# Optimization experiments

Measured on AMD Instinct MI355X. Metric: run time of the kernel, lower is better.

The kernel has to match this reference:

```python
import jax, jax.numpy as jnp
import numpy as np

B, T, E, H, NH = 8, 1024, 128, 1024, 16
HD = H // NH  # head dim = 64

def _split_heads(x):
    # [B, S, H] -> [B, NH, S, HD]
    b, s, _ = x.shape
    return x.reshape(b, s, NH, HD).transpose(0, 2, 1, 3)

def setup_inputs() -> dict:
    key = jax.random.key(0)
    ks = jax.random.split(key, 16)
    std = 0.02
    inp = {
        "token_hidden_states": jax.random.normal(ks[0], (B, T, H), jnp.float32),
        "entity_hidden_states": jax.random.normal(ks[1], (B, E, H), jnp.float32),
        "attention_mask": jnp.zeros((B, 1, 1, T + E), jnp.float32),
        "query_pos": jax.random.normal(ks[2], (B, E, H), jnp.float32),
        # word q/k/v projections
        "Wq": jax.random.normal(ks[3], (H, H), jnp.float32) * std,
        "bq": jnp.zeros((H,), jnp.float32),
        "Wk": jax.random.normal(ks[4], (H, H), jnp.float32) * std,
        "bk": jnp.zeros((H,), jnp.float32),
        "Wv": jax.random.normal(ks[5], (H, H), jnp.float32) * std,
        "bv": jnp.zeros((H,), jnp.float32),
        # entity-aware e2w q/k/v projections
        "Weq": jax.random.normal(ks[6], (H, H), jnp.float32) * std,
        "beq": jnp.zeros((H,), jnp.float32),
        "Wek": jax.random.normal(ks[7], (H, H), jnp.float32) * std,
        "bek": jnp.zeros((H,), jnp.float32),
        "Wev": jax.random.normal(ks[8], (H, H), jnp.float32) * std,
        "bev": jnp.zeros((H,), jnp.float32),
    }
    return inp

def reference(token_hidden_states, entity_hidden_states, attention_mask, query_pos,
              Wq, bq, Wk, bk, Wv, bv, Weq, beq, Wek, bek, Wev, bev):
    tok = token_hidden_states
    ent = entity_hidden_states
    pos_ent = (ent + query_pos) * 0.5  # pos-aware entity states

    # projections (entity-aware branch uses separate weights; e2w value uses raw ent)
    w2w_q = _split_heads(tok @ Wq.T + bq)       # [B,NH,T,HD]
    e2w_q = _split_heads(pos_ent @ Weq.T + beq) # [B,NH,E,HD]
    w2w_k = _split_heads(tok @ Wk.T + bk)
    e2w_k = _split_heads(pos_ent @ Wek.T + bek)
    w2w_v = _split_heads(tok @ Wv.T + bv)
    e2w_v = _split_heads(ent @ Wev.T + bev)

    # The four-block score matrix [[w2w, w2e],[e2w, e2e]] equals one matmul of
    # concatenated query/key streams along the sequence axis.
    q = jnp.concatenate([w2w_q, e2w_q], axis=2)  # [B,NH,T+E,HD]
    k = jnp.concatenate([w2w_k, e2w_k], axis=2)
    v = jnp.concatenate([w2w_v, e2w_v], axis=2)

    scores = jnp.einsum("bhqd,bhkd->bhqk", q, k) / np.sqrt(HD).astype(np.float32)
    scores = scores + attention_mask
    probs = jax.nn.softmax(scores, axis=-1)  # dropout prob = 0 -> identity
    ctx = jnp.einsum("bhqk,bhkd->bhqd", probs, v)  # [B,NH,T+E,HD]

    # merge heads -> [B, T+E, H]
    ctx = ctx.transpose(0, 2, 1, 3).reshape(tok.shape[0], T + E, NH * HD)
    return ctx[:, :T, :], ctx[:, T:, :]

if __name__ == "__main__":
    out = reference(**setup_inputs())
    print(out[0].shape, out[1].shape)
```

## Files before the change

### kernel.cpp

```cpp
#include <hip/hip_runtime.h>
#include <cstdint>


typedef __attribute__((ext_vector_type(8))) short s16x8;
typedef __attribute__((ext_vector_type(4))) float f32x4;
typedef __attribute__((ext_vector_type(4))) unsigned short u16x4;
typedef __attribute__((ext_vector_type(2))) unsigned int u32x2;

#define DEVFN static __device__ __forceinline__

DEVFN unsigned short f2bf(float f) {
  uint32_t u = __builtin_bit_cast(uint32_t, f);
  u += 0x7fffu + ((u >> 16) & 1u);
  return (unsigned short)(u >> 16);
}

DEVFN uint32_t pk_bf16(float lo, float hi) {
  uint32_t r;
  asm("v_cvt_pk_bf16_f32 %0, %1, %2" : "=v"(r) : "v"(lo), "v"(hi));
  return r;
}

DEVFN float vexp2(float x) {
  float r;
  asm("v_exp_f32 %0, %1" : "=v"(r) : "v"(x));
  return r;
}

DEVFN void gload16(const void* g, void* lds) {
  using GP = const __attribute__((address_space(1))) uint32_t*;
  using LP = __attribute__((address_space(3))) uint32_t*;
  __builtin_amdgcn_global_load_lds(
      reinterpret_cast<GP>(reinterpret_cast<uintptr_t>(g)),
      reinterpret_cast<LP>((uint32_t)reinterpret_cast<uintptr_t>(lds)),
      16, 0, 0);
}

__global__ __launch_bounds__(256) void prep_kernel(
    const float* __restrict__ tok, const float* __restrict__ ent,
    const float* __restrict__ qpos,
    const float* __restrict__ W0, const float* __restrict__ W1,
    const float* __restrict__ W2, const float* __restrict__ W3,
    const float* __restrict__ W4, const float* __restrict__ W5,
    unsigned short* __restrict__ dst)
{
  const int NG = 4194304;
  for (int g = blockIdx.x * blockDim.x + threadIdx.x; g < NG;
       g += gridDim.x * blockDim.x) {
    int e = g << 2;
    f32x4 v;
    if (e < 8388608) {
      v = *(const f32x4*)(tok + e);
    } else if (e < 9437184) {
      int i = e - 8388608;
      f32x4 a = *(const f32x4*)(ent + i);
      f32x4 p = *(const f32x4*)(qpos + i);
      v = (a + p) * 0.5f;
    } else if (e < 10485760) {
      v = *(const f32x4*)(ent + (e - 9437184));
    } else {
      int i = e - 10485760;
      int wsel = i >> 20;
      const float* W = wsel == 0 ? W0 : wsel == 1 ? W1 : wsel == 2 ? W2
                     : wsel == 3 ? W3 : wsel == 4 ? W4 : W5;
      v = *(const f32x4*)(W + (i & 1048575));
    }
    u16x4 o;
#pragma unroll
    for (int j = 0; j < 4; ++j) o[j] = f2bf(v[j]);
    *(u16x4*)(dst + e) = o;
  }
}

__global__ __launch_bounds__(256) void proj_gemm(
    const unsigned short* __restrict__ Atok, const unsigned short* __restrict__ Ape,
    const unsigned short* __restrict__ Aent, const unsigned short* __restrict__ Wb6,
    const float* __restrict__ b0, const float* __restrict__ b1,
    const float* __restrict__ b2, const float* __restrict__ b3,
    const float* __restrict__ b4, const float* __restrict__ b5,
    unsigned short* __restrict__ Qo, unsigned short* __restrict__ Ko,
    unsigned short* __restrict__ Vt)
{
  __shared__ __align__(16) unsigned short As[2][2][4096];
  __shared__ __align__(16) unsigned short Bs[2][2][4096];

  const int tid = threadIdx.x;
  const int l = tid & 63, w = tid >> 6;
  const int lr = l & 15, lg = l >> 4;
  const int bx = blockIdx.x, by = blockIdx.y;
  const int which = bx >> 3;
  const int n0l = (bx & 7) << 7;
  const bool entm = by >= 64;
  const int byl = entm ? by - 64 : by;
  const int wsel = which + (entm ? 3 : 0);
  const unsigned short* A = entm ? (which == 2 ? Aent : Ape) : Atok;
  const unsigned short* Wp = Wb6 + (size_t)wsel * 1048576;
  const float* bias = entm ? (which == 0 ? b3 : which == 1 ? b4 : b5)
                           : (which == 0 ? b0 : which == 1 ? b1 : b2);
  const int bShift = entm ? 7 : 10;
  const int sBase = entm ? 1024 : 0;
  const float qscale = (which == 0) ? 0.125f * 1.44269504088896f : 1.0f;

  const int c0 = w * 2, c1 = w * 2 + 1;
  const int sr0 = c0 * 16 + (l >> 2), sr1 = c1 * 16 + (l >> 2);
  const int sc0 = ((l & 3) * 8) ^ (((sr0 >> 1) & 3) << 3);
  const int sc1 = ((l & 3) * 8) ^ (((sr1 >> 1) & 3) << 3);
  const unsigned short* gA0 = A + (size_t)(byl * 128 + sr0) * 1024 + sc0;
  const unsigned short* gA1 = A + (size_t)(byl * 128 + sr1) * 1024 + sc1;
  const unsigned short* gB0 = Wp + (size_t)(n0l + sr0) * 1024 + sc0;
  const unsigned short* gB1 = Wp + (size_t)(n0l + sr1) * 1024 + sc1;

  const int wr = w >> 1, wc = w & 1;
  int offA[4], offB[4];
#pragma unroll
  for (int mi = 0; mi < 4; ++mi) {
    int row = wr * 64 + mi * 16 + lr;
    offA[mi] = row * 32 + ((lg * 8) ^ (((row >> 1) & 3) << 3));
  }
#pragma unroll
  for (int ni = 0; ni < 4; ++ni) {
    int row = wc * 64 + ni * 16 + lr;
    offB[ni] = row * 32 + ((lg * 8) ^ (((row >> 1) & 3) << 3));
  }

  auto STAGE = [&](int kt, int bi) {
#pragma unroll
    for (int s = 0; s < 2; ++s) {
      const int ko = kt * 64 + s * 32;
      gload16(gA0 + ko, &As[bi][s][c0 * 512]);
      gload16(gA1 + ko, &As[bi][s][c1 * 512]);
      gload16(gB0 + ko, &Bs[bi][s][c0 * 512]);
      gload16(gB1 + ko, &Bs[bi][s][c1 * 512]);
    }
  };

  auto COMPUTE = [&](int cur, f32x4 (&acc)[4][4]) {
#pragma unroll
    for (int s = 0; s < 2; ++s) {
      s16x8 a[4], b[4];
#pragma unroll
      for (int mi = 0; mi < 4; ++mi) a[mi] = *(const s16x8*)(&As[cur][s][offA[mi]]);
#pragma unroll
      for (int ni = 0; ni < 4; ++ni) b[ni] = *(const s16x8*)(&Bs[cur][s][offB[ni]]);
#pragma unroll
      for (int mi = 0; mi < 4; ++mi)
#pragma unroll
        for (int ni = 0; ni < 4; ++ni)
          acc[mi][ni] = __builtin_amdgcn_mfma_f32_16x16x32_bf16(
              a[mi], b[ni], acc[mi][ni], 0, 0, 0);
    }
  };

  f32x4 acc[4][4] = {};
  STAGE(0, 0);
  STAGE(1, 1);
  for (int kt = 0; kt < 15; ++kt) {
    const int cur = kt & 1;
    asm volatile("s_waitcnt vmcnt(8)" ::: "memory");
    __builtin_amdgcn_s_barrier();
    COMPUTE(cur, acc);
    __builtin_amdgcn_s_barrier();
    if (kt + 2 < 16) STAGE(kt + 2, cur);
  }
  {
    asm volatile("s_waitcnt vmcnt(0)" ::: "memory");
    __builtin_amdgcn_s_barrier();
    COMPUTE(15 & 1, acc);
  }

  const int bMask = (1 << bShift) - 1;
#pragma unroll
  for (int mi = 0; mi < 4; ++mi) {
    const int i0 = byl * 128 + wr * 64 + mi * 16 + lg * 4;
#pragma unroll
    for (int ni = 0; ni < 4; ++ni) {
      const int j = n0l + wc * 64 + ni * 16 + lr;
      const float bv = bias[j];
      const int h = j >> 6, d = j & 63;
      if (which < 2) {
        unsigned short* dst = (which == 0) ? Qo : Ko;
#pragma unroll
        for (int r = 0; r < 4; ++r) {
          const int i = i0 + r;
          const int bidx = i >> bShift;
          const int s = sBase + (i & bMask);
          dst[((size_t)(bidx * 16 + h) * 1152 + s) * 64 + d] =
              f2bf((acc[mi][ni][r] + bv) * qscale);
        }
      } else {
        const int bidx = i0 >> bShift;
        const int s0 = sBase + (i0 & bMask);
        u16x4 pk;
#pragma unroll
        for (int r = 0; r < 4; ++r) pk[r] = f2bf(acc[mi][ni][r] + bv);
        *(u16x4*)(Vt + ((size_t)(bidx * 16 + h) * 64 + d) * 1152 + s0) = pk;
      }
    }
  }
}

__global__ __launch_bounds__(256) void attn_kernel(
    const unsigned short* __restrict__ Q, const unsigned short* __restrict__ K,
    const unsigned short* __restrict__ Vt, const float* __restrict__ mask,
    float* __restrict__ out)
{
  __shared__ __align__(16) unsigned short Klds[2][4096];
  __shared__ __align__(16) unsigned short Vlds[2][4096];
  __shared__ __align__(16) unsigned short Plds[4][2048];
  const int tid = threadIdx.x, l = tid & 63, w = tid >> 6;
  const int c = l & 15, g = l >> 4;
  const int nblk = blockIdx.x;
  const int xcd = nblk & 7, jj = nblk >> 3;
  const int qt = jj % 9;
  const int bh = (jj / 9) * 8 + xcd;
  const int b = bh >> 4, h = bh & 15;
  const unsigned short* Qh = Q + (size_t)bh * 73728;
  const unsigned short* Kh = K + (size_t)bh * 73728;
  const unsigned short* Vh = Vt + (size_t)bh * 73728;
  const float* mrow = mask + b * 1152;
  const int q0 = qt * 128 + w * 32;
  const f32x4 fz = {0.f, 0.f, 0.f, 0.f};
  char* Pw = (char*)&Plds[w][0];
  const int swz = (c & 7) << 4;
  const float LOG2E = 1.44269504088896f;

  const int rsub = l >> 3;
  const int ksw8 = ((l & 7) ^ rsub) << 3;
  const int ccA = w * 2, ccB = w * 2 + 1;
  const int rA = ccA * 8 + rsub, rB = ccB * 8 + rsub;
  const int q1 = (g ^ (c & 7)) << 3;
  const int q2 = ((g + 4) ^ (c & 7)) << 3;

  s16x8 ones;
#pragma unroll
  for (int j = 0; j < 8; ++j) ones[j] = (short)0x3F80;

  s16x8 qb[2][2];
#pragma unroll
  for (int mi = 0; mi < 2; ++mi)
#pragma unroll
    for (int ds = 0; ds < 2; ++ds)
      qb[mi][ds] =
          *(const s16x8*)(Qh + (size_t)(q0 + mi * 16 + c) * 64 + ds * 32 + g * 8);

  f32x4 OT[2][4] = {};
  f32x4 den[2] = {};

  auto STAGE = [&](int tt, int bi) {
    const int kv0 = tt * 64;
    gload16(Kh + (size_t)(kv0 + rA) * 64 + ksw8, &Klds[bi][ccA * 512]);
    gload16(Kh + (size_t)(kv0 + rB) * 64 + ksw8, &Klds[bi][ccB * 512]);
    gload16(Vh + (size_t)rA * 1152 + kv0 + ksw8, &Vlds[bi][ccA * 512]);
    gload16(Vh + (size_t)rB * 1152 + kv0 + ksw8, &Vlds[bi][ccB * 512]);
  };

  STAGE(0, 0);
  for (int t = 0; t < 18; ++t) {
    const int kv0 = t * 64;
    const int cur = t & 1;
    __syncthreads();

    f32x4 mv[4];
#pragma unroll
    for (int ni = 0; ni < 4; ++ni)
      mv[ni] = *(const f32x4*)(mrow + kv0 + ni * 16 + g * 4) * LOG2E;

    if (t + 1 < 18) STAGE(t + 1, cur ^ 1);

    f32x4 st[2][4];
#pragma unroll
    for (int ni = 0; ni < 4; ++ni) {
      const unsigned short* kp = &Klds[cur][(ni * 16 + c) * 64];
      s16x8 ka0 = *(const s16x8*)(kp + q1);
      s16x8 ka1 = *(const s16x8*)(kp + q2);
#pragma unroll
      for (int mi = 0; mi < 2; ++mi) {
        f32x4 tq = __builtin_amdgcn_mfma_f32_16x16x32_bf16(ka0, qb[mi][0], fz, 0, 0, 0);
        tq = __builtin_amdgcn_mfma_f32_16x16x32_bf16(ka1, qb[mi][1], tq, 0, 0, 0);
        st[mi][ni] = tq + mv[ni];
      }
    }

#pragma unroll
    for (int mi = 0; mi < 2; ++mi)
#pragma unroll
      for (int ni = 0; ni < 4; ++ni)
#pragma unroll
        for (int r = 0; r < 4; ++r)
          st[mi][ni][r] = vexp2(st[mi][ni][r]);

#pragma unroll
    for (int mi = 0; mi < 2; ++mi)
#pragma unroll
      for (int ni = 0; ni < 4; ++ni) {
        u32x2 dd = {pk_bf16(st[mi][ni][0], st[mi][ni][1]),
                    pk_bf16(st[mi][ni][2], st[mi][ni][3])};
        const int off = (mi * 16 + c) * 128 + ((ni * 32 + g * 8) ^ swz);
        *(u32x2*)(Pw + off) = dd;
      }

    s16x8 pb[2][2];
#pragma unroll
    for (int mi = 0; mi < 2; ++mi)
#pragma unroll
      for (int ks = 0; ks < 2; ++ks)
        pb[mi][ks] =
            *(const s16x8*)(Pw + (mi * 16 + c) * 128 + ((ks * 64 + g * 16) ^ swz));

#pragma unroll
    for (int di = 0; di < 4; ++di) {
      const unsigned short* vp = &Vlds[cur][(di * 16 + c) * 64];
      s16x8 va0 = *(const s16x8*)(vp + q1);
      s16x8 va1 = *(const s16x8*)(vp + q2);
#pragma unroll
      for (int mi = 0; mi < 2; ++mi) {
        OT[mi][di] =
            __builtin_amdgcn_mfma_f32_16x16x32_bf16(va0, pb[mi][0], OT[mi][di], 0, 0, 0);
        OT[mi][di] =
            __builtin_amdgcn_mfma_f32_16x16x32_bf16(va1, pb[mi][1], OT[mi][di], 0, 0, 0);
      }
    }
#pragma unroll
    for (int mi = 0; mi < 2; ++mi) {
      den[mi] = __builtin_amdgcn_mfma_f32_16x16x32_bf16(ones, pb[mi][0], den[mi], 0, 0, 0);
      den[mi] = __builtin_amdgcn_mfma_f32_16x16x32_bf16(ones, pb[mi][1], den[mi], 0, 0, 0);
    }
  }

  float* obase;
  if (q0 < 1024) {
    obase = out + ((size_t)(b * 1024 + q0) * 1024 + h * 64);
  } else {
    obase = out + 8388608u + ((size_t)(b * 128 + (q0 - 1024)) * 1024 + h * 64);
  }
  float inv[2] = {1.0f / den[0][0], 1.0f / den[1][0]};
#pragma unroll
  for (int mi = 0; mi < 2; ++mi)
#pragma unroll
    for (int di = 0; di < 4; ++di) {
      f32x4 v = OT[mi][di] * inv[mi];
      *(f32x4*)(obase + (size_t)(mi * 16 + c) * 1024 + di * 16 + g * 4) = v;
    }
}

extern "C" void kernel_launch(void* const* d_in, const int* in_sizes, int n_in,
                              void* d_out, int out_size, void* d_ws, size_t ws_size,
                              hipStream_t stream) {
  const float* tok  = (const float*)d_in[0];
  const float* ent  = (const float*)d_in[1];
  const float* mask = (const float*)d_in[2];
  const float* qpos = (const float*)d_in[3];
  const float* Wq  = (const float*)d_in[4];  const float* bq  = (const float*)d_in[5];
  const float* Wk  = (const float*)d_in[6];  const float* bk  = (const float*)d_in[7];
  const float* Wv  = (const float*)d_in[8];  const float* bv  = (const float*)d_in[9];
  const float* Weq = (const float*)d_in[10]; const float* beq = (const float*)d_in[11];
  const float* Wek = (const float*)d_in[12]; const float* bek = (const float*)d_in[13];
  const float* Wev = (const float*)d_in[14]; const float* bev = (const float*)d_in[15];
  float* out = (float*)d_out;

  unsigned short* ws = (unsigned short*)d_ws;
  unsigned short* tokBF = ws;
  unsigned short* peBF  = ws + 8388608;
  unsigned short* entBF = ws + 9437184;
  unsigned short* WBF   = ws + 10485760;
  unsigned short* Qb    = ws + 16777216;
  unsigned short* Kb    = ws + 26214400;
  unsigned short* Vtb   = ws + 35651584;

  prep_kernel<<<2048, 256, 0, stream>>>(tok, ent, qpos, Wq, Wk, Wv, Weq, Wek, Wev, ws);
  proj_gemm<<<dim3(24, 72), 256, 0, stream>>>(tokBF, peBF, entBF, WBF,
                                              bq, bk, bv, beq, bek, bev,
                                              Qb, Kb, Vtb);
  attn_kernel<<<1152, 256, 0, stream>>>(Qb, Kb, Vtb, mask, out);
}
```

Before: 168.1 us.

## Fuse Q/K/V projections into one block sharing the staged A tile

Each proj_gemm block now computes the Q, K and V output tiles together, loading the activation tile once and reusing it across all three weight matrices. The grid shrinks from 24x72 to 8x72 blocks, and the K-step drops to 32 with three accumulator sets per thread. The entity path also stages a second A tile (raw entity) for V. This reduces redundant A loads and launches, but it triples accumulator registers (192 fp32), which can cut occupancy. It also leaves fewer blocks to fill the GPU.

```diff
diff --git a/kernel.cpp b/kernel.cpp
--- a/kernel.cpp
+++ b/kernel.cpp
@@ -1,5 +1,6 @@
 #include <hip/hip_runtime.h>
 #include <cstdint>
+#include <type_traits>
 
 
 typedef __attribute__((ext_vector_type(8))) short s16x8;
@@ -81,34 +82,42 @@
     unsigned short* __restrict__ Qo, unsigned short* __restrict__ Ko,
     unsigned short* __restrict__ Vt)
 {
-  __shared__ __align__(16) unsigned short As[2][2][4096];
-  __shared__ __align__(16) unsigned short Bs[2][2][4096];
+  __shared__ __align__(16) unsigned short T[2][5][4096];
 
   const int tid = threadIdx.x;
   const int l = tid & 63, w = tid >> 6;
   const int lr = l & 15, lg = l >> 4;
   const int bx = blockIdx.x, by = blockIdx.y;
-  const int which = bx >> 3;
-  const int n0l = (bx & 7) << 7;
+  const int n0l = bx << 7;
   const bool entm = by >= 64;
   const int byl = entm ? by - 64 : by;
-  const int wsel = which + (entm ? 3 : 0);
-  const unsigned short* A = entm ? (which == 2 ? Aent : Ape) : Atok;
-  const unsigned short* Wp = Wb6 + (size_t)wsel * 1048576;
-  const float* bias = entm ? (which == 0 ? b3 : which == 1 ? b4 : b5)
-                           : (which == 0 ? b0 : which == 1 ? b1 : b2);
+  const unsigned short* A  = entm ? Ape  : Atok;
+  const unsigned short* A2 = entm ? Aent : Atok;
+  const unsigned short* Wq = Wb6 + (size_t)(entm ? 3 : 0) * 1048576;
+  const unsigned short* Wk = Wb6 + (size_t)(entm ? 4 : 1) * 1048576;
+  const unsigned short* Wv = Wb6 + (size_t)(entm ? 5 : 2) * 1048576;
+  const float* biasq = entm ? b3 : b0;
+  const float* biask = entm ? b4 : b1;
+  const float* biasv = entm ? b5 : b2;
   const int bShift = entm ? 7 : 10;
   const int sBase = entm ? 1024 : 0;
-  const float qscale = (which == 0) ? 0.125f * 1.44269504088896f : 1.0f;
+  const float QSC = 0.125f * 1.44269504088896f;
 
   const int c0 = w * 2, c1 = w * 2 + 1;
   const int sr0 = c0 * 16 + (l >> 2), sr1 = c1 * 16 + (l >> 2);
   const int sc0 = ((l & 3) * 8) ^ (((sr0 >> 1) & 3) << 3);
   const int sc1 = ((l & 3) * 8) ^ (((sr1 >> 1) & 3) << 3);
-  const unsigned short* gA0 = A + (size_t)(byl * 128 + sr0) * 1024 + sc0;
-  const unsigned short* gA1 = A + (size_t)(byl * 128 + sr1) * 1024 + sc1;
-  const unsigned short* gB0 = Wp + (size_t)(n0l + sr0) * 1024 + sc0;
-  const unsigned short* gB1 = Wp + (size_t)(n0l + sr1) * 1024 + sc1;
+  const size_t ro0 = (size_t)(byl * 128 + sr0) * 1024, ro1 = (size_t)(byl * 128 + sr1) * 1024;
+  const unsigned short* gA0  = A  + ro0 + sc0;
+  const unsigned short* gA1  = A  + ro1 + sc1;
+  const unsigned short* gA20 = A2 + ro0 + sc0;
+  const unsigned short* gA21 = A2 + ro1 + sc1;
+  const unsigned short* gBq0 = Wq + (size_t)(n0l + sr0) * 1024 + sc0;
+  const unsigned short* gBq1 = Wq + (size_t)(n0l + sr1) * 1024 + sc1;
+  const unsigned short* gBk0 = Wk + (size_t)(n0l + sr0) * 1024 + sc0;
+  const unsigned short* gBk1 = Wk + (size_t)(n0l + sr1) * 1024 + sc1;
+  const unsigned short* gBv0 = Wv + (size_t)(n0l + sr0) * 1024 + sc0;
+  const unsigned short* gBv1 = Wv + (size_t)(n0l + sr1) * 1024 + sc1;
 
   const int wr = w >> 1, wc = w & 1;
   int offA[4], offB[4];
@@ -123,78 +132,117 @@
     offB[ni] = row * 32 + ((lg * 8) ^ (((row >> 1) & 3) << 3));
   }
 
-  auto STAGE = [&](int kt, int bi) {
-#pragma unroll
-    for (int s = 0; s < 2; ++s) {
-      const int ko = kt * 64 + s * 32;
-      gload16(gA0 + ko, &As[bi][s][c0 * 512]);
-      gload16(gA1 + ko, &As[bi][s][c1 * 512]);
-      gload16(gB0 + ko, &Bs[bi][s][c0 * 512]);
-      gload16(gB1 + ko, &Bs[bi][s][c1 * 512]);
-    }
-  };
-
-  auto COMPUTE = [&](int cur, f32x4 (&acc)[4][4]) {
-#pragma unroll
-    for (int s = 0; s < 2; ++s) {
+  f32x4 accq[4][4] = {}, acck[4][4] = {}, accv[4][4] = {};
+
+  auto RUN = [&](auto EC) {
+    constexpr bool EN = decltype(EC)::value;
+    auto STAGE = [&](int kt, int bi) {
+      const int ko = kt * 32;
+      gload16(gA0 + ko,  &T[bi][0][c0 * 512]);
+      gload16(gA1 + ko,  &T[bi][0][c1 * 512]);
+      gload16(gBq0 + ko, &T[bi][1][c0 * 512]);
+      gload16(gBq1 + ko, &T[bi][1][c1 * 512]);
+      gload16(gBk0 + ko, &T[bi][2][c0 * 512]);
+      gload16(gBk1 + ko, &T[bi][2][c1 * 512]);
+      gload16(gBv0 + ko, &T[bi][3][c0 * 512]);
+      gload16(gBv1 + ko, &T[bi][3][c1 * 512]);
+      if constexpr (EN) {
+        gload16(gA20 + ko, &T[bi][4][c0 * 512]);
+        gload16(gA21 + ko, &T[bi][4][c1 * 512]);
+      }
+    };
+    auto COMPUTE = [&](int cur) {
       s16x8 a[4], b[4];
 #pragma unroll
-      for (int mi = 0; mi < 4; ++mi) a[mi] = *(const s16x8*)(&As[cur][s][offA[mi]]);
-#pragma unroll
-      for (int ni = 0; ni < 4; ++ni) b[ni] = *(const s16x8*)(&Bs[cur][s][offB[ni]]);
+      for (int mi = 0; mi < 4; ++mi) a[mi] = *(const s16x8*)(&T[cur][0][offA[mi]]);
+#pragma unroll
+      for (int ni = 0; ni < 4; ++ni) b[ni] = *(const s16x8*)(&T[cur][1][offB[ni]]);
 #pragma unroll
       for (int mi = 0; mi < 4; ++mi)
 #pragma unroll
         for (int ni = 0; ni < 4; ++ni)
-          acc[mi][ni] = __builtin_amdgcn_mfma_f32_16x16x32_bf16(
-              a[mi], b[ni], acc[mi][ni], 0, 0, 0);
-    }
-  };
-
-  f32x4 acc[4][4] = {};
-  STAGE(0, 0);
-  STAGE(1, 1);
-  for (int kt = 0; kt < 15; ++kt) {
-    const int cur = kt & 1;
-    asm volatile("s_waitcnt vmcnt(8)" ::: "memory");
-    __builtin_amdgcn_s_barrier();
-    COMPUTE(cur, acc);
-    __builtin_amdgcn_s_barrier();
-    if (kt + 2 < 16) STAGE(kt + 2, cur);
-  }
-  {
+          accq[mi][ni] = __builtin_amdgcn_mfma_f32_16x16x32_bf16(
+              a[mi], b[ni], accq[mi][ni], 0, 0, 0);
+#pragma unroll
+      for (int ni = 0; ni < 4; ++ni) b[ni] = *(const s16x8*)(&T[cur][2][offB[ni]]);
+#pragma unroll
+      for (int mi = 0; mi < 4; ++mi)
+#pragma unroll
+        for (int ni = 0; ni < 4; ++ni)
+          acck[mi][ni] = __builtin_amdgcn_mfma_f32_16x16x32_bf16(
+              a[mi], b[ni], acck[mi][ni], 0, 0, 0);
+      if constexpr (EN) {
+#pragma unroll
+        for (int mi = 0; mi < 4; ++mi) a[mi] = *(const s16x8*)(&T[cur][4][offA[mi]]);
+      }
+#pragma unroll
+      for (int ni = 0; ni < 4; ++ni) b[ni] = *(const s16x8*)(&T[cur][3][offB[ni]]);
+#pragma unroll
+      for (int mi = 0; mi < 4; ++mi)
+#pragma unroll
+        for (int ni = 0; ni < 4; ++ni)
+          accv[mi][ni] = __builtin_amdgcn_mfma_f32_16x16x32_bf16(
+              a[mi], b[ni], accv[mi][ni], 0, 0, 0);
+    };
+
+    STAGE(0, 0);
+    STAGE(1, 1);
+    for (int kt = 0; kt < 31; ++kt) {
+      const int cur = kt & 1;
+      if constexpr (EN)
+        asm volatile("s_waitcnt vmcnt(10)" ::: "memory");
+      else
+        asm volatile("s_waitcnt vmcnt(8)" ::: "memory");
+      __builtin_amdgcn_s_barrier();
+      COMPUTE(cur);
+      __builtin_amdgcn_s_barrier();
+      if (kt + 2 < 32) STAGE(kt + 2, cur);
+    }
     asm volatile("s_waitcnt vmcnt(0)" ::: "memory");
     __builtin_amdgcn_s_barrier();
-    COMPUTE(15 & 1, acc);
-  }
+    COMPUTE(1);
+  };
+  if (entm) RUN(std::integral_constant<bool, true>{});
+  else      RUN(std::integral_constant<bool, false>{});
 
   const int bMask = (1 << bShift) - 1;
-#pragma unroll
-  for (int mi = 0; mi < 4; ++mi) {
-    const int i0 = byl * 128 + wr * 64 + mi * 16 + lg * 4;
-#pragma unroll
-    for (int ni = 0; ni < 4; ++ni) {
-      const int j = n0l + wc * 64 + ni * 16 + lr;
-      const float bv = bias[j];
-      const int h = j >> 6, d = j & 63;
-      if (which < 2) {
-        unsigned short* dst = (which == 0) ? Qo : Ko;
+  auto EPQK = [&](f32x4 (&acc)[4][4], const float* bias, unsigned short* dst,
+                  float scale) {
+#pragma unroll
+    for (int mi = 0; mi < 4; ++mi) {
+      const int i0 = byl * 128 + wr * 64 + mi * 16 + lg * 4;
+#pragma unroll
+      for (int ni = 0; ni < 4; ++ni) {
+        const int j = n0l + wc * 64 + ni * 16 + lr;
+        const float bv = bias[j];
+        const int h = j >> 6, d = j & 63;
 #pragma unroll
         for (int r = 0; r < 4; ++r) {
           const int i = i0 + r;
           const int bidx = i >> bShift;
           const int s = sBase + (i & bMask);
           dst[((size_t)(bidx * 16 + h) * 1152 + s) * 64 + d] =
-              f2bf((acc[mi][ni][r] + bv) * qscale);
+              f2bf((acc[mi][ni][r] + bv) * scale);
         }
-      } else {
-        const int bidx = i0 >> bShift;
-        const int s0 = sBase + (i0 & bMask);
-        u16x4 pk;
-#pragma unroll
-        for (int r = 0; r < 4; ++r) pk[r] = f2bf(acc[mi][ni][r] + bv);
-        *(u16x4*)(Vt + ((size_t)(bidx * 16 + h) * 64 + d) * 1152 + s0) = pk;
-      }
+      }
+    }
+  };
+  EPQK(accq, biasq, Qo, QSC);
+  EPQK(acck, biask, Ko, 1.0f);
+#pragma unroll
+  for (int mi = 0; mi < 4; ++mi) {
+    const int i0 = byl * 128 + wr * 64 + mi * 16 + lg * 4;
+    const int bidx = i0 >> bShift;
+    const int s0 = sBase + (i0 & bMask);
+#pragma unroll
+    for (int ni = 0; ni < 4; ++ni) {
+      const int j = n0l + wc * 64 + ni * 16 + lr;
+      const float bv = biasv[j];
+      const int h = j >> 6, d = j & 63;
+      u16x4 pk;
+#pragma unroll
+      for (int r = 0; r < 4; ++r) pk[r] = f2bf(accv[mi][ni][r] + bv);
+      *(u16x4*)(Vt + ((size_t)(bidx * 16 + h) * 64 + d) * 1152 + s0) = pk;
     }
   }
 }
@@ -368,8 +416,8 @@
   unsigned short* Vtb   = ws + 35651584;
 
   prep_kernel<<<2048, 256, 0, stream>>>(tok, ent, qpos, Wq, Wk, Wv, Weq, Wek, Wev, ws);
-  proj_gemm<<<dim3(24, 72), 256, 0, stream>>>(tokBF, peBF, entBF, WBF,
-                                              bq, bk, bv, beq, bek, bev,
-                                              Qb, Kb, Vtb);
+  proj_gemm<<<dim3(8, 72), 256, 0, stream>>>(tokBF, peBF, entBF, WBF,
+                                             bq, bk, bv, beq, bek, bev,
+                                             Qb, Kb, Vtb);
   attn_kernel<<<1152, 256, 0, stream>>>(Qb, Kb, Vtb, mask, out);
 }
```

New measurement: 193.0 us. +14.8%, slower.
